# Optimization experiments

Measured on AMD Instinct MI355X. Metric: run time of the kernel, lower is better.

Reference implementation:

```python
import jax, jax.numpy as jnp
import numpy as np
from jax.scipy.special import logsumexp

V = 100000      # vocab_size
D = 256         # embedding_dim
HID = 512       # hidden_dim (bidirectional concat)
H = HID // 2    # per-direction LSTM hidden
S = 4096        # seq_len
T = 12          # tagset_size
A = 128         # attention_dim
START, STOP = 10, 11
NEG = -10000.0


def setup_inputs() -> dict:
    key = jax.random.key(0)
    ks = jax.random.split(key, 20)
    sc = 0.05
    n = lambda k, shp: jax.random.normal(k, shp, dtype=jnp.float32) * sc
    transitions = jax.random.normal(ks[16], (T, T), dtype=jnp.float32)
    transitions = transitions.at[START, :].set(NEG).at[:, STOP].set(NEG)
    return {
        "sentence": jax.random.randint(ks[0], (S,), 0, V),
        "tags": jax.random.randint(ks[1], (S,), 0, 10),
        "embed": n(ks[2], (V, D)),
        # LSTM layer 0 (input D), per direction [fwd, bwd]; PyTorch gate order i,f,g,o
        "lstm0_Wih": n(ks[3], (2, 4 * H, D)),
        "lstm0_Whh": n(ks[4], (2, 4 * H, H)),
        "lstm0_b": n(ks[5], (2, 4 * H)),
        # LSTM layer 1 (input HID = concat of both directions)
        "lstm1_Wih": n(ks[6], (2, 4 * H, HID)),
        "lstm1_Whh": n(ks[7], (2, 4 * H, H)),
        "lstm1_b": n(ks[8], (2, 4 * H)),
        # attention
        "Wa": n(ks[9], (A, HID)),
        "ba": n(ks[10], (A,)),
        "v_ctx": n(ks[11], (A,)),
        # hidden2tag MLP: Linear(HID, HID//2) -> ReLU -> Linear(HID//2, T)
        "W1": n(ks[12], (HID // 2, HID)),
        "b1": n(ks[13], (HID // 2,)),
        "W2": n(ks[14], (T, HID // 2)),
        "b2": n(ks[15], (T,)),
        "transitions": transitions,
    }


def _bilstm(x, Wih, Whh, b):
    """x: (S, in_dim) -> (S, 2H). Dropout is eval-mode identity."""
    def run(dirn):
        Wi, Wh, bb = Wih[dirn], Whh[dirn], b[dirn]
        def step(carry, xt):
            h, c = carry
            g = xt @ Wi.T + h @ Wh.T + bb           # (4H,)
            i, f, gg, o = jnp.split(g, 4)
            i, f, o = jax.nn.sigmoid(i), jax.nn.sigmoid(f), jax.nn.sigmoid(o)
            c = f * c + i * jnp.tanh(gg)
            h = o * jnp.tanh(c)
            return (h, c), h
        init = (jnp.zeros((H,), x.dtype), jnp.zeros((H,), x.dtype))
        _, hs = jax.lax.scan(step, init, x, reverse=(dirn == 1))
        return hs
    return jnp.concatenate([run(0), run(1)], axis=-1)


def reference(sentence, tags, embed, lstm0_Wih, lstm0_Whh, lstm0_b,
              lstm1_Wih, lstm1_Whh, lstm1_b, Wa, ba, v_ctx,
              W1, b1, W2, b2, transitions):
    # --- features: embed -> 2-layer BiLSTM -> attention reweight -> MLP ---
    x = embed[sentence]                                  # (S, D)
    h = _bilstm(x, lstm0_Wih, lstm0_Whh, lstm0_b)        # (S, HID)
    h = _bilstm(h, lstm1_Wih, lstm1_Whh, lstm1_b)        # (S, HID)
    scores = jnp.tanh(h @ Wa.T + ba) @ v_ctx             # (S,)
    w = jax.nn.softmax(scores, axis=0)                   # softmax over seq (dim=0)
    h = h * w[:, None]
    feats = jax.nn.relu(h @ W1.T + b1) @ W2.T + b2       # (S, T) emissions

    # --- CRF forward algorithm (log partition) ---
    fv0 = jnp.full((T,), NEG, feats.dtype).at[START].set(0.0)
    def crf_step(fv, feat):
        return logsumexp(fv[None, :] + transitions, axis=1) + feat, None
    fv, _ = jax.lax.scan(crf_step, fv0, feats)
    forward_score = logsumexp(fv + transitions[STOP])

    # --- gold path score ---
    tws = jnp.concatenate([jnp.array([START], dtype=tags.dtype), tags])
    trans_sc = transitions[tws[1:], tws[:-1]].sum()
    emit_sc = feats[jnp.arange(S), tags].sum()
    gold_score = trans_sc + emit_sc + transitions[STOP, tags[-1]]

    return (forward_score - gold_score)[None]             # (1,) NLL
```

## Files before the change

kernel.cpp:

```cpp
#include <hip/hip_runtime.h>
#include <math.h>

#define SEQ 4096
#define DIM 256
#define HIDD 512
#define HH 256
#define G4 1024
#define TT 12
#define AA 128
#define START_TAG 10
#define STOP_TAG 11
#define NEGV (-10000.0f)
#define NG 4
#define SL 64
#define NC 64
#define CL 64

typedef unsigned int u32;
typedef unsigned long long u64;

__device__ __forceinline__ float sigf(float x){ return 1.0f/(1.0f+__expf(-x)); }
__device__ __forceinline__ float tanhfast(float x){ float e=__expf(2.f*x); return (e-1.f)/(e+1.f); }

__device__ __forceinline__ unsigned short f2bf(float f){
  u32 u = __float_as_uint(f);
  u32 r = u + 0x7fffu + ((u>>16)&1u);
  return (unsigned short)(r>>16);
}

template<int K>
__global__ __launch_bounds__(256) void pack_wih(const float* __restrict__ src, float4* __restrict__ dst){
  const int KQ = K/4;
  int idx = blockIdx.x*256 + threadIdx.x;
  int j = idx & (G4-1);
  int r = idx >> 10;
  int k4 = r % KQ;
  int d  = r / KQ;
  const float* p = src + ((size_t)(d*G4 + j))*K + k4*4;
  dst[idx] = make_float4(p[0],p[1],p[2],p[3]);
}

__global__ __launch_bounds__(256) void pack_whh(const float* __restrict__ src, uint4* __restrict__ dst){
  int idx = blockIdx.x*256 + threadIdx.x;
  int j  = idx & (G4-1);
  int k8 = (idx>>10) & 31;
  int d  = idx >> 15;
  const float* p = src + ((size_t)(d*G4 + j))*HH + k8*8;
  uint4 v;
  v.x = (u32)f2bf(p[0]) | ((u32)f2bf(p[1])<<16);
  v.y = (u32)f2bf(p[2]) | ((u32)f2bf(p[3])<<16);
  v.z = (u32)f2bf(p[4]) | ((u32)f2bf(p[5])<<16);
  v.w = (u32)f2bf(p[6]) | ((u32)f2bf(p[7])<<16);
  dst[idx] = v;
}

__global__ __launch_bounds__(64) void gather_embed(const int* __restrict__ sent, const float* __restrict__ embed,
                                                   float4* __restrict__ x4){
  int s = blockIdx.x;
  const float4* src = (const float4*)(embed + (size_t)sent[s]*DIM);
  x4[(size_t)s*64 + threadIdx.x] = src[threadIdx.x];
}

template<int K>
__global__ __launch_bounds__(256) void inproj(const float* __restrict__ in, const float4* __restrict__ WT4,
                                              const float* __restrict__ bias, float* __restrict__ P){
  const int KQ = K/4;
  int bid = blockIdx.x;
  int jt = bid & 3;
  int st = (bid>>2) & 255;
  int d  = bid >> 10;
  __shared__ float4 xs[16*KQ];
  int tid = threadIdx.x;
  int s0 = st*16;
  const float4* in4 = (const float4*)(in + (size_t)s0*K);
  for (int i=tid; i<16*KQ; i+=256) xs[i] = in4[i];
  __syncthreads();
  int j = jt*256 + tid;
  float b = bias[d*G4 + j];
  float acc[16];
  #pragma unroll
  for (int r=0;r<16;r++) acc[r]=b;
  const float4* w = WT4 + (size_t)d*KQ*G4 + j;
  for (int k4=0;k4<KQ;k4++){
    float4 wv = w[(size_t)k4*G4];
    #pragma unroll
    for (int r=0;r<16;r++){
      float4 xv = xs[r*KQ + k4];
      acc[r] = fmaf(wv.x,xv.x, fmaf(wv.y,xv.y, fmaf(wv.z,xv.z, fmaf(wv.w,xv.w, acc[r]))));
    }
  }
  #pragma unroll
  for (int r=0;r<16;r++)
    P[((size_t)d*SEQ + (s0+r))*G4 + j] = acc[r];
}

#define QDOT(i,A) { uint4 qv = wl[(i)*256 + tid]; \
  float4 ha = hs4[2*(i)]; float4 hb = hs4[2*(i)+1]; \
  A = fmaf(__uint_as_float(qv.x<<16),           ha.x, A); \
  A = fmaf(__uint_as_float(qv.x & 0xffff0000u), ha.y, A); \
  A = fmaf(__uint_as_float(qv.y<<16),           ha.z, A); \
  A = fmaf(__uint_as_float(qv.y & 0xffff0000u), ha.w, A); \
  A = fmaf(__uint_as_float(qv.z<<16),           hb.x, A); \
  A = fmaf(__uint_as_float(qv.z & 0xffff0000u), hb.y, A); \
  A = fmaf(__uint_as_float(qv.w<<16),           hb.z, A); \
  A = fmaf(__uint_as_float(qv.w & 0xffff0000u), hb.w, A); }

__global__ __launch_bounds__(256,1) void lstm_scan7(const uint4* __restrict__ WhhB,
                                                    const float* __restrict__ P,
                                                    float* __restrict__ hout,
                                                    u64* __restrict__ exbase){
  extern __shared__ uint4 smem[];
  uint4*  wl  = smem;
  float4* hs4 = (float4*)(wl + 32*256);
  float*  gv  = (float*)(hs4 + 64);
  float*  hs  = (float*)hs4;

  const int d = blockIdx.x & 1;
  const int g = blockIdx.x >> 1;
  const int tid = threadIdx.x;
  const int q  = tid >> 6;
  const int jj = tid & 63;
  const int j  = q*256 + g*SL + jj;

  const uint4* wsrc = WhhB + (size_t)d*32*G4 + j;
  #pragma unroll 4
  for (int k8=0;k8<32;k8++) wl[k8*256 + tid] = wsrc[(size_t)k8*G4];

  hs[tid] = 0.f;
  float c = 0.f;
  const float* Pd = P + (size_t)d*SEQ*G4;
  const int t0 = d ? SEQ-1 : 0;
  float pcur = Pd[(size_t)t0*G4 + j];
  u64* exd = exbase + (size_t)d*1024;
  __syncthreads();

  for (int tt=0; tt<SEQ; ++tt){
    const int t  = d ? (SEQ-1-tt) : tt;
    const int tn = d ? (t>0 ? t-1 : 0) : (t<SEQ-1 ? t+1 : t);
    float pnext = Pd[(size_t)tn*G4 + j];

    float acc0 = pcur, acc1 = 0.f, acc2 = 0.f, acc3 = 0.f;
    #pragma unroll
    for (int kk=0; kk<8; ++kk){
      QDOT(kk*4+0,acc0) QDOT(kk*4+1,acc1) QDOT(kk*4+2,acc2) QDOT(kk*4+3,acc3)
    }
    gv[tid] = (acc0+acc1)+(acc2+acc3);
    __syncthreads();

    u64* exsl = exd + (size_t)(tt&3)*256;
    if (tid < SL){
      float gi = sigf(gv[tid]);
      float gf = sigf(gv[64 + tid]);
      float gg = tanhfast(gv[128 + tid]);
      float go = sigf(gv[192 + tid]);
      c = gf*c + gi*gg;
      float h = go*tanhfast(c);
      hout[(size_t)t*HIDD + d*HH + g*SL + tid] = h;
      u64 pk = ((u64)(u32)(tt+1) << 32) | (u64)__float_as_uint(h);
      __hip_atomic_store(&exsl[g*SL + tid], pk, __ATOMIC_RELAXED, __HIP_MEMORY_SCOPE_AGENT);
    }
    const u64 want = (u64)(u32)(tt+1);
    u64 v;
    do {
      v = __hip_atomic_load(&exsl[tid], __ATOMIC_RELAXED, __HIP_MEMORY_SCOPE_AGENT);
    } while ((v>>32) != want);
    hs[tid] = __uint_as_float((u32)v);
    pcur = pnext;
    __syncthreads();
  }
}

__global__ __launch_bounds__(128) void attn_scores(const float* __restrict__ h1, const float* __restrict__ Wa,
                                                   const float* __restrict__ ba, const float* __restrict__ vctx,
                                                   float* __restrict__ scores){
  __shared__ float4 hsl[8*128];
  __shared__ float red[2];
  int tid = threadIdx.x;
  int s0 = blockIdx.x*8;
  const float4* h4 = (const float4*)(h1 + (size_t)s0*HIDD);
  for (int i=tid;i<8*128;i+=128) hsl[i]=h4[i];
  __syncthreads();
  const float4* wa = (const float4*)(Wa + (size_t)tid*HIDD);
  float acc[8];
  #pragma unroll
  for (int r=0;r<8;r++) acc[r]=0.f;
  for (int k4=0;k4<128;k4++){
    float4 wv = wa[k4];
    #pragma unroll
    for (int r=0;r<8;r++){
      float4 xv = hsl[r*128+k4];
      acc[r] = fmaf(wv.x,xv.x,fmaf(wv.y,xv.y,fmaf(wv.z,xv.z,fmaf(wv.w,xv.w,acc[r]))));
    }
  }
  float myb = ba[tid], myv = vctx[tid];
  for (int r=0;r<8;r++){
    float p = tanhf(acc[r]+myb)*myv;
    #pragma unroll
    for (int off=32;off;off>>=1) p += __shfl_down(p, off);
    if ((tid&63)==0) red[tid>>6]=p;
    __syncthreads();
    if (tid==0) scores[s0+r] = red[0]+red[1];
    __syncthreads();
  }
}

__global__ __launch_bounds__(1024) void softmax_seq(const float* __restrict__ scores, float* __restrict__ wsm){
  __shared__ float red[16];
  __shared__ float gsh[2];
  int tid=threadIdx.x;
  float4 v = ((const float4*)scores)[tid];
  float m = fmaxf(fmaxf(v.x,v.y),fmaxf(v.z,v.w));
  #pragma unroll
  for (int off=32;off;off>>=1) m = fmaxf(m, __shfl_down(m,off));
  if ((tid&63)==0) red[tid>>6]=m;
  __syncthreads();
  if (tid==0){ float mm=red[0]; for (int i=1;i<16;i++) mm=fmaxf(mm,red[i]); gsh[0]=mm; }
  __syncthreads();
  float gm = gsh[0];
  float e0=__expf(v.x-gm), e1=__expf(v.y-gm), e2=__expf(v.z-gm), e3=__expf(v.w-gm);
  float s = e0+e1+e2+e3;
  #pragma unroll
  for (int off=32;off;off>>=1) s += __shfl_down(s,off);
  if ((tid&63)==0) red[tid>>6]=s;
  __syncthreads();
  if (tid==0){ float ss=0; for (int i=0;i<16;i++) ss+=red[i]; gsh[1]=ss; }
  __syncthreads();
  float inv = 1.0f/gsh[1];
  ((float4*)wsm)[tid] = make_float4(e0*inv,e1*inv,e2*inv,e3*inv);
}

__global__ __launch_bounds__(256) void mlp_feats(const float* __restrict__ h1, const float* __restrict__ wsm,
                                                 const float* __restrict__ W1, const float* __restrict__ b1,
                                                 const float* __restrict__ W2, const float* __restrict__ b2,
                                                 float* __restrict__ feats){
  __shared__ float4 hsl[8*128];
  __shared__ float rl[8][256];
  __shared__ float wloc[8];
  int tid=threadIdx.x;
  int s0=blockIdx.x*8;
  const float4* h4=(const float4*)(h1 + (size_t)s0*HIDD);
  for (int i=tid;i<8*128;i+=256) hsl[i]=h4[i];
  if (tid<8) wloc[tid]=wsm[s0+tid];
  __syncthreads();
  const float4* w1=(const float4*)(W1 + (size_t)tid*HIDD);
  float acc[8];
  #pragma unroll
  for (int r=0;r<8;r++) acc[r]=0.f;
  for (int k4=0;k4<128;k4++){
    float4 wv=w1[k4];
    #pragma unroll
    for (int r=0;r<8;r++){
      float4 xv=hsl[r*128+k4];
      acc[r]=fmaf(wv.x,xv.x,fmaf(wv.y,xv.y,fmaf(wv.z,xv.z,fmaf(wv.w,xv.w,acc[r]))));
    }
  }
  float bb=b1[tid];
  #pragma unroll
  for (int r=0;r<8;r++) rl[r][tid]=fmaxf(fmaf(acc[r],wloc[r],bb),0.f);
  __syncthreads();
  if (tid < 96){
    int r=tid/12, t=tid-12*(tid/12);
    const float* w2=W2 + t*256;
    float a=b2[t];
    for (int m2=0;m2<256;m2++) a += w2[m2]*rl[r][m2];
    feats[(size_t)(s0+r)*TT + t]=a;
  }
}

__global__ __launch_bounds__(192) void crf_chunks(const float* __restrict__ feats,
                                                  const float* __restrict__ trans,
                                                  float* __restrict__ Cmat){
  int c = blockIdx.x;
  int tid = threadIdx.x;
  __shared__ float trs[144];
  __shared__ float cur[144];
  __shared__ float ft[12];
  if (tid<144) trs[tid]=trans[tid];
  __syncthreads();
  int t0 = c*CL;
  int i = tid/12, jcol = tid - 12*(tid/12);
  float cv = 0.f;
  if (tid<144) cv = trs[tid] + feats[(size_t)t0*TT + i];
  for (int s=t0+1; s<t0+CL; ++s){
    if (tid<144) cur[tid]=cv;
    if (tid<12)  ft[tid] = feats[(size_t)s*TT+tid];
    __syncthreads();
    if (tid<144){
      float v[12]; float m=-3.0e38f;
      #pragma unroll
      for (int k=0;k<12;k++){ v[k] = trs[i*12+k] + cur[k*12+jcol]; m=fmaxf(m,v[k]); }
      float ss=0.f;
      #pragma unroll
      for (int k=0;k<12;k++) ss += __expf(v[k]-m);
      cv = ft[i] + m + __logf(ss);
    }
    __syncthreads();
  }
  if (tid<144) Cmat[(size_t)c*144 + tid] = cv;
}

__global__ __launch_bounds__(256) void crf_combine(const float* __restrict__ Cmat,
                                                   const float* __restrict__ trans,
                                                   const float* __restrict__ feats,
                                                   const int* __restrict__ tags,
                                                   float* __restrict__ out){
  __shared__ float trb[144];
  __shared__ float fv[12];
  __shared__ float Csh[144];
  __shared__ float red[4];
  __shared__ float goldsh;
  int tid=threadIdx.x;
  if (tid<144) trb[tid]=trans[tid];
  __syncthreads();
  float gacc=0.f;
  for (int s=tid; s<SEQ; s+=256){
    int tg = tags[s];
    int pv = s ? tags[s-1] : START_TAG;
    gacc += feats[(size_t)s*TT+tg] + trb[tg*12+pv];
  }
  #pragma unroll
  for (int off=32;off;off>>=1) gacc += __shfl_down(gacc,off);
  if ((tid&63)==0) red[tid>>6]=gacc;
  __syncthreads();
  if (tid==0) goldsh = red[0]+red[1]+red[2]+red[3] + trb[STOP_TAG*12 + tags[SEQ-1]];
  if (tid<12) fv[tid] = (tid==START_TAG) ? 0.f : NEGV;
  __syncthreads();
  for (int cc=0; cc<NC; ++cc){
    if (tid<144) Csh[tid] = Cmat[(size_t)cc*144+tid];
    __syncthreads();
    float nf=0.f;
    if (tid<12){
      float v[12]; float m=-3.0e38f;
      #pragma unroll
      for (int k=0;k<12;k++){ v[k]=Csh[tid*12+k]+fv[k]; m=fmaxf(m,v[k]); }
      float ss=0.f;
      #pragma unroll
      for (int k=0;k<12;k++) ss+=__expf(v[k]-m);
      nf = m+__logf(ss);
    }
    __syncthreads();
    if (tid<12) fv[tid]=nf;
    __syncthreads();
  }
  if (tid==0){
    float v[12]; float m=-3.0e38f;
    #pragma unroll
    for (int k=0;k<12;k++){ v[k]=fv[k]+trb[STOP_TAG*12+k]; m=fmaxf(m,v[k]); }
    float ss=0.f;
    #pragma unroll
    for (int k=0;k<12;k++) ss+=__expf(v[k]-m);
    out[0] = m + __logf(ss) - goldsh;
  }
}

extern "C" void kernel_launch(void* const* d_in, const int* in_sizes, int n_in,
                              void* d_out, int out_size, void* d_ws, size_t ws_size,
                              hipStream_t stream){
  const int*   sent  = (const int*)d_in[0];
  const int*   tags  = (const int*)d_in[1];
  const float* embed = (const float*)d_in[2];
  const float* W0ih  = (const float*)d_in[3];
  const float* W0hh  = (const float*)d_in[4];
  const float* b0    = (const float*)d_in[5];
  const float* W1ih  = (const float*)d_in[6];
  const float* W1hh  = (const float*)d_in[7];
  const float* b1l   = (const float*)d_in[8];
  const float* Wa    = (const float*)d_in[9];
  const float* ba    = (const float*)d_in[10];
  const float* vctx  = (const float*)d_in[11];
  const float* W1m   = (const float*)d_in[12];
  const float* b1m   = (const float*)d_in[13];
  const float* W2m   = (const float*)d_in[14];
  const float* b2m   = (const float*)d_in[15];
  const float* trans = (const float*)d_in[16];
  float* out = (float*)d_out;

  float* ws = (float*)d_ws;
  size_t off = 0;
  float*  x     = ws + off;            off += (size_t)SEQ*DIM;
  float4* WihT0 = (float4*)(ws + off); off += (size_t)2*64*G4*4;
  float4* WihT1 = (float4*)(ws + off); off += (size_t)2*128*G4*4;
  uint4*  WhhB0 = (uint4*)(ws + off);  off += (size_t)2*32*G4*4;
  uint4*  WhhB1 = (uint4*)(ws + off);  off += (size_t)2*32*G4*4;
  float*  h0    = ws + off;            off += (size_t)SEQ*HIDD;
  float*  h1    = ws + off;            off += (size_t)SEQ*HIDD;
  float*  scores= ws + off;            off += SEQ;
  float*  wsm   = ws + off;            off += SEQ;
  float*  feats = ws + off;            off += (size_t)SEQ*TT;
  float*  Cmat  = ws + off;            off += (size_t)NC*144;
  u64*    exch  = (u64*)(ws + off);    off += (size_t)2*2048*2;
  float*  P     = ws + off;            off += (size_t)2*SEQ*G4;

  const int scanLds = 32*256*16 + 64*16 + 256*4;
  hipFuncSetAttribute((const void*)lstm_scan7, hipFuncAttributeMaxDynamicSharedMemorySize, scanLds);

  pack_wih<256><<<dim3(2*64*G4/256), dim3(256), 0, stream>>>(W0ih, WihT0);
  pack_wih<512><<<dim3(2*128*G4/256), dim3(256), 0, stream>>>(W1ih, WihT1);
  pack_whh<<<dim3(2*32*G4/256), dim3(256), 0, stream>>>(W0hh, WhhB0);
  pack_whh<<<dim3(2*32*G4/256), dim3(256), 0, stream>>>(W1hh, WhhB1);

  gather_embed<<<dim3(SEQ), dim3(64), 0, stream>>>(sent, embed, (float4*)x);

  inproj<256><<<dim3(2048), dim3(256), 0, stream>>>(x, WihT0, b0, P);
  lstm_scan7<<<dim3(2*NG), dim3(256), scanLds, stream>>>(WhhB0, P, h0, exch);
  inproj<512><<<dim3(2048), dim3(256), 0, stream>>>(h0, WihT1, b1l, P);
  lstm_scan7<<<dim3(2*NG), dim3(256), scanLds, stream>>>(WhhB1, P, h1, exch + 2048);

  attn_scores<<<dim3(512), dim3(128), 0, stream>>>(h1, Wa, ba, vctx, scores);
  softmax_seq<<<dim3(1), dim3(1024), 0, stream>>>(scores, wsm);
  mlp_feats<<<dim3(512), dim3(256), 0, stream>>>(h1, wsm, W1m, b1m, W2m, b2m, feats);
  crf_chunks<<<dim3(NC), dim3(192), 0, stream>>>(feats, trans, Cmat);
  crf_combine<<<dim3(1), dim3(256), 0, stream>>>(Cmat, trans, feats, tags, out);
}
```

Measured before the change: 24.89 ms.

## Overlap remote hidden-state exchange with local recurrent dot-product slice

Each LSTM scan block now writes its own hidden slice straight to shared memory and begins the recurrent matvec on that local slice. Meanwhile it issues the load for the other blocks' slices from the previous step's exchange buffer and spins only after the local work is done. The point is to hide cross-block exchange latency behind compute on the serial critical path. __syncthreads is also replaced with a bare s_waitcnt plus s_barrier; the exchange now relies on a 4-slot ring with relaxed atomics, so correctness depends on ordering assumptions.

```diff
diff --git a/kernel.cpp b/kernel.cpp
--- a/kernel.cpp
+++ b/kernel.cpp
@@ -22,6 +22,13 @@
 __device__ __forceinline__ float sigf(float x){ return 1.0f/(1.0f+__expf(-x)); }
 __device__ __forceinline__ float tanhfast(float x){ float e=__expf(2.f*x); return (e-1.f)/(e+1.f); }
 
+__device__ __forceinline__ void lds_barrier(){
+  asm volatile("s_waitcnt lgkmcnt(0)" ::: "memory");
+  __builtin_amdgcn_sched_barrier(0);
+  __builtin_amdgcn_s_barrier();
+  __builtin_amdgcn_sched_barrier(0);
+}
+
 __device__ __forceinline__ unsigned short f2bf(float f){
   u32 u = __float_as_uint(f);
   u32 r = u + 0x7fffu + ((u>>16)&1u);
@@ -105,7 +112,7 @@
   A = fmaf(__uint_as_float(qv.w<<16),           hb.z, A); \
   A = fmaf(__uint_as_float(qv.w & 0xffff0000u), hb.w, A); }
 
-__global__ __launch_bounds__(256,1) void lstm_scan7(const uint4* __restrict__ WhhB,
+__global__ __launch_bounds__(256,1) void lstm_scan8(const uint4* __restrict__ WhhB,
                                                     const float* __restrict__ P,
                                                     float* __restrict__ hout,
                                                     u64* __restrict__ exbase){
@@ -121,6 +128,7 @@
   const int q  = tid >> 6;
   const int jj = tid & 63;
   const int j  = q*256 + g*SL + jj;
+  const bool remote = (tid>>6) != g;
 
   const uint4* wsrc = WhhB + (size_t)d*32*G4 + j;
   #pragma unroll 4
@@ -139,15 +147,36 @@
     const int tn = d ? (t>0 ? t-1 : 0) : (t<SEQ-1 ? t+1 : t);
     float pnext = Pd[(size_t)tn*G4 + j];
 
+    u64* expl = exd + (size_t)((tt+3)&3)*256;
+    const u64 want = (u64)(u32)tt;
+    u64 v = 0;
+    if (tt>0 && remote)
+      v = __hip_atomic_load(&expl[tid], __ATOMIC_RELAXED, __HIP_MEMORY_SCOPE_AGENT);
+
     float acc0 = pcur, acc1 = 0.f, acc2 = 0.f, acc3 = 0.f;
-    #pragma unroll
-    for (int kk=0; kk<8; ++kk){
-      QDOT(kk*4+0,acc0) QDOT(kk*4+1,acc1) QDOT(kk*4+2,acc2) QDOT(kk*4+3,acc3)
+    {
+      const int kb = g*8;
+      QDOT(kb+0,acc0) QDOT(kb+1,acc1) QDOT(kb+2,acc2) QDOT(kb+3,acc3)
+      QDOT(kb+4,acc0) QDOT(kb+5,acc1) QDOT(kb+6,acc2) QDOT(kb+7,acc3)
+    }
+
+    if (tt>0 && remote){
+      while ((v>>32) != want)
+        v = __hip_atomic_load(&expl[tid], __ATOMIC_RELAXED, __HIP_MEMORY_SCOPE_AGENT);
+      hs[tid] = __uint_as_float((u32)v);
+    }
+    lds_barrier();
+
+    #pragma unroll
+    for (int rg=1; rg<4; ++rg){
+      const int kb = ((g+rg)&3)*8;
+      QDOT(kb+0,acc0) QDOT(kb+1,acc1) QDOT(kb+2,acc2) QDOT(kb+3,acc3)
+      QDOT(kb+4,acc0) QDOT(kb+5,acc1) QDOT(kb+6,acc2) QDOT(kb+7,acc3)
     }
     gv[tid] = (acc0+acc1)+(acc2+acc3);
-    __syncthreads();
-
-    u64* exsl = exd + (size_t)(tt&3)*256;
+    lds_barrier();
+
+    u64* exst = exd + (size_t)(tt&3)*256;
     if (tid < SL){
       float gi = sigf(gv[tid]);
       float gf = sigf(gv[64 + tid]);
@@ -155,18 +184,13 @@
       float go = sigf(gv[192 + tid]);
       c = gf*c + gi*gg;
       float h = go*tanhfast(c);
+      hs[g*SL + tid] = h;
+      u64 pk = ((u64)(u32)(tt+1) << 32) | (u64)__float_as_uint(h);
+      __hip_atomic_store(&exst[g*SL + tid], pk, __ATOMIC_RELAXED, __HIP_MEMORY_SCOPE_AGENT);
       hout[(size_t)t*HIDD + d*HH + g*SL + tid] = h;
-      u64 pk = ((u64)(u32)(tt+1) << 32) | (u64)__float_as_uint(h);
-      __hip_atomic_store(&exsl[g*SL + tid], pk, __ATOMIC_RELAXED, __HIP_MEMORY_SCOPE_AGENT);
-    }
-    const u64 want = (u64)(u32)(tt+1);
-    u64 v;
-    do {
-      v = __hip_atomic_load(&exsl[tid], __ATOMIC_RELAXED, __HIP_MEMORY_SCOPE_AGENT);
-    } while ((v>>32) != want);
-    hs[tid] = __uint_as_float((u32)v);
+    }
     pcur = pnext;
-    __syncthreads();
+    lds_barrier();
   }
 }
 
@@ -392,7 +416,7 @@
   float*  P     = ws + off;            off += (size_t)2*SEQ*G4;
 
   const int scanLds = 32*256*16 + 64*16 + 256*4;
-  hipFuncSetAttribute((const void*)lstm_scan7, hipFuncAttributeMaxDynamicSharedMemorySize, scanLds);
+  hipFuncSetAttribute((const void*)lstm_scan8, hipFuncAttributeMaxDynamicSharedMemorySize, scanLds);
 
   pack_wih<256><<<dim3(2*64*G4/256), dim3(256), 0, stream>>>(W0ih, WihT0);
   pack_wih<512><<<dim3(2*128*G4/256), dim3(256), 0, stream>>>(W1ih, WihT1);
@@ -402,9 +426,9 @@
   gather_embed<<<dim3(SEQ), dim3(64), 0, stream>>>(sent, embed, (float4*)x);
 
   inproj<256><<<dim3(2048), dim3(256), 0, stream>>>(x, WihT0, b0, P);
-  lstm_scan7<<<dim3(2*NG), dim3(256), scanLds, stream>>>(WhhB0, P, h0, exch);
+  lstm_scan8<<<dim3(2*NG), dim3(256), scanLds, stream>>>(WhhB0, P, h0, exch);
   inproj<512><<<dim3(2048), dim3(256), 0, stream>>>(h0, WihT1, b1l, P);
-  lstm_scan7<<<dim3(2*NG), dim3(256), scanLds, stream>>>(WhhB1, P, h1, exch + 2048);
+  lstm_scan8<<<dim3(2*NG), dim3(256), scanLds, stream>>>(WhhB1, P, h1, exch + 2048);
 
   attn_scores<<<dim3(512), dim3(128), 0, stream>>>(h1, Wa, ba, vctx, scores);
   softmax_seq<<<dim3(1), dim3(1024), 0, stream>>>(scores, wsm);
```

Result: faster. 21.65 ms (-13.0%).
